# Kernel optimization log

Measured on AMD Instinct MI355X. Metric: run time of the kernel, lower is better.

Reference implementation:

```python
import jax, jax.numpy as jnp
import numpy as np
import math

INF = 10000000000.0
D_KEY = 64


def setup_inputs() -> dict:
    key = jax.random.key(0)
    kq, kk, kv = jax.random.split(key, 3)
    B, S, D = 4, 4096, D_KEY
    return {
        "query": jax.random.normal(kq, (B, S, D), dtype=jnp.float32),
        "key": jax.random.normal(kk, (B, S, D), dtype=jnp.float32),
        "value": jax.random.normal(kv, (B, S, D), dtype=jnp.float32),
    }


def reference(query, key, value):
    # dot_products: [B, Sq, Sk]
    scale = math.sqrt(D_KEY)
    scores = jnp.einsum("bqd,bkd->bqk", query, key)
    S = key.shape[1]
    # causal: subtract INF on strict upper triangle (triu(1)), before scaling
    tri = jnp.triu(jnp.full((S, S), INF, dtype=scores.dtype), k=1)
    scores = scores - tri[None, :, :]
    logits = scores / scale
    probs = jax.nn.softmax(logits, axis=-1)  # softmax over key dim
    # dropout p=0.0 -> identity
    return jnp.einsum("bqk,bkd->bqd", probs, value)
```

## Files before the change

### kernel.cpp

```cpp
#include <hip/hip_runtime.h>
#include <hip/hip_bf16.h>
#include <math.h>

#define B_  4
#define S_  4096
#define D_  64
#define NQT 64
#define NST 32
#define LDP 68
#define QSC 0.18033688f
#define M0  20.0f

typedef __attribute__((ext_vector_type(8))) short bf16x8;
typedef __attribute__((ext_vector_type(4))) float f32x4;
typedef __attribute__((ext_vector_type(4))) short short4v;

static __device__ inline short f2bf(float f) {
    union { float f; unsigned u; } v; v.f = f;
    unsigned u = v.u;
    unsigned r = u + 0x7fff + ((u >> 16) & 1);
    return (short)(r >> 16);
}
static __device__ inline float bf2f(short s) {
    union { unsigned u; float f; } v; v.u = ((unsigned)(unsigned short)s) << 16;
    return v.f;
}

__global__ __launch_bounds__(256) void fa_prep(const float* __restrict__ K,
                                               const float* __restrict__ V,
                                               short* __restrict__ Kbf,
                                               short* __restrict__ Vtbf)
{
    const int b   = blockIdx.x >> 6;
    const int st  = blockIdx.x & 63;
    const int tid = threadIdx.x;
    __shared__ short Vs[64 * 72];

    const size_t tbase = ((size_t)b * S_ + (size_t)st * 64) * D_;
    #pragma unroll
    for (int rr = 0; rr < 4; ++rr) {
        int i = tid + rr * 256;
        size_t e = tbase + (size_t)i * 4;
        f32x4 k = *(const f32x4*)(K + e);
        short4v ks;
        ks[0] = f2bf(k[0]); ks[1] = f2bf(k[1]);
        ks[2] = f2bf(k[2]); ks[3] = f2bf(k[3]);
        *(short4v*)(Kbf + e) = ks;
        f32x4 v = *(const f32x4*)(V + e);
        int key = i >> 4, d4 = (i & 15) * 4;
        Vs[(d4 + 0) * 72 + key] = f2bf(v[0]);
        Vs[(d4 + 1) * 72 + key] = f2bf(v[1]);
        Vs[(d4 + 2) * 72 + key] = f2bf(v[2]);
        Vs[(d4 + 3) * 72 + key] = f2bf(v[3]);
    }
    __syncthreads();
    #pragma unroll
    for (int cc = 0; cc < 2; ++cc) {
        int c = tid + cc * 256;
        int d = c >> 3, sg = c & 7;
        bf16x8 row = *(const bf16x8*)&Vs[d * 72 + sg * 8];
        *(bf16x8*)(Vtbf + ((size_t)(b * D_ + d)) * S_ + (size_t)st * 64 + sg * 8) = row;
    }
}

__global__ __launch_bounds__(512) void fa_part(const float* __restrict__ Qf,
                                               const short* __restrict__ Kbf,
                                               const short* __restrict__ Vtbf,
                                               short* __restrict__ Opart,
                                               float* __restrict__ Lpart,
                                               int CH, int T)
{
    const int bid = blockIdx.x;
    const int b   = bid / T;
    int r = bid - b * T;
    int qt2 = NST - 1;
    while (true) {
        int n = (2 * qt2 + 2 + CH - 1) / CH;
        if (r < n) break;
        r -= n; --qt2;
    }
    const int kt0 = r * CH;
    const int nkt = 2 * qt2 + 2;
    const int kt1 = (kt0 + CH < nkt) ? kt0 + CH : nkt;

    const int tid  = threadIdx.x;
    const int wave = tid >> 6;
    const int lane = tid & 63;
    const int lm   = lane & 15;
    const int lk   = lane >> 4;

    __shared__ __align__(16) short Ks[64 * 64];
    __shared__ __align__(16) short Vt[64 * 64];
    __shared__ __align__(16) short Ps[128 * LDP];

    bf16x8 qA[2];
    {
        const float* qp = Qf + ((size_t)(b * S_ + qt2 * 128 + wave * 16 + lm)) * D_;
        #pragma unroll
        for (int h = 0; h < 2; ++h) {
            f32x4 a0 = *(const f32x4*)(qp + h * 32 + lk * 8);
            f32x4 a1 = *(const f32x4*)(qp + h * 32 + lk * 8 + 4);
            qA[h][0] = f2bf(a0[0] * QSC); qA[h][1] = f2bf(a0[1] * QSC);
            qA[h][2] = f2bf(a0[2] * QSC); qA[h][3] = f2bf(a0[3] * QSC);
            qA[h][4] = f2bf(a1[0] * QSC); qA[h][5] = f2bf(a1[1] * QSC);
            qA[h][6] = f2bf(a1[2] * QSC); qA[h][7] = f2bf(a1[3] * QSC);
        }
    }

    const int srow = tid >> 3;
    const int sseg = (tid & 7) ^ (srow & 7);
    const char* kgp = (const char*)(Kbf + (size_t)b * S_ * D_)
                    + (size_t)(kt0 * 64 + srow) * 128 + sseg * 16;
    const char* vgp = (const char*)(Vtbf + ((size_t)(b * D_ + srow)) * S_)
                    + (size_t)kt0 * 128 + sseg * 16;

    bf16x8 kreg = *(const bf16x8*)kgp;
    bf16x8 vreg = *(const bf16x8*)vgp;
    kgp += 8192; vgp += 128;

    float l_i[4] = {0.f, 0.f, 0.f, 0.f};
    f32x4 o_acc[4];
    #pragma unroll
    for (int dt = 0; dt < 4; ++dt) o_acc[dt] = (f32x4){0.f, 0.f, 0.f, 0.f};

    const int wrow = wave * 16 + lk * 4;

    for (int kt = kt0; kt < kt1; ++kt) {
        __syncthreads();
        *(bf16x8*)&Ks[tid * 8] = kreg;
        *(bf16x8*)&Vt[tid * 8] = vreg;
        __syncthreads();

        if (kt + 1 < kt1) {
            kreg = *(const bf16x8*)kgp;
            vreg = *(const bf16x8*)vgp;
            kgp += 8192; vgp += 128;
        }

        f32x4 s4[4];
        #pragma unroll
        for (int ct = 0; ct < 4; ++ct) {
            f32x4 acc = (f32x4){0.f, 0.f, 0.f, 0.f};
            #pragma unroll
            for (int h = 0; h < 2; ++h) {
                int seg = (h * 4 + lk) ^ (lm & 7);
                bf16x8 bF = *(const bf16x8*)&Ks[(ct * 16 + lm) * 64 + seg * 8];
                acc = __builtin_amdgcn_mfma_f32_16x16x32_bf16(qA[h], bF, acc, 0, 0, 0);
            }
            s4[ct] = acc;
        }

        if (kt >= 2 * qt2) {
            const int koff = kt * 64 - qt2 * 128;
            #pragma unroll
            for (int ct = 0; ct < 4; ++ct) {
                #pragma unroll
                for (int rr = 0; rr < 4; ++rr) {
                    if (koff + ct * 16 + lm > wrow + rr) s4[ct][rr] = -INFINITY;
                }
            }
        }

        #pragma unroll
        for (int ct = 0; ct < 4; ++ct) {
            #pragma unroll
            for (int rr = 0; rr < 4; ++rr) {
                float p = exp2f(s4[ct][rr] - M0);
                s4[ct][rr] = p;
                l_i[rr] += p;
            }
        }
        #pragma unroll
        for (int ct = 0; ct < 4; ++ct) {
            #pragma unroll
            for (int rr = 0; rr < 4; ++rr) {
                Ps[(wrow + rr) * LDP + ct * 16 + lm] = f2bf(s4[ct][rr]);
            }
        }
        bf16x8 aF[2];
        #pragma unroll
        for (int kh = 0; kh < 2; ++kh)
            aF[kh] = *(const bf16x8*)&Ps[(wave * 16 + lm) * LDP + kh * 32 + lk * 8];
        #pragma unroll
        for (int dt = 0; dt < 4; ++dt) {
            #pragma unroll
            for (int kh = 0; kh < 2; ++kh) {
                int seg = (kh * 4 + lk) ^ (lm & 7);
                bf16x8 bF = *(const bf16x8*)&Vt[(dt * 16 + lm) * 64 + seg * 8];
                o_acc[dt] = __builtin_amdgcn_mfma_f32_16x16x32_bf16(aF[kh], bF, o_acc[dt], 0, 0, 0);
            }
        }
    }

    short* Op = Opart + (size_t)bid * (128 * D_);
    #pragma unroll
    for (int rr = 0; rr < 4; ++rr) {
        float rs = l_i[rr];
        rs += __shfl_xor(rs, 1);
        rs += __shfl_xor(rs, 2);
        rs += __shfl_xor(rs, 4);
        rs += __shfl_xor(rs, 8);
        int row = wrow + rr;
        #pragma unroll
        for (int dt = 0; dt < 4; ++dt)
            Op[row * D_ + dt * 16 + lm] = f2bf(o_acc[dt][rr]);
        if (lm == 0) Lpart[(size_t)bid * 128 + row] = rs;
    }
}

__global__ __launch_bounds__(256) void fa_combine(const short* __restrict__ Opart,
                                                  const float* __restrict__ Lpart,
                                                  float* __restrict__ O,
                                                  int CH, int T)
{
    const int idx = blockIdx.x * 256 + threadIdx.x;
    const int b   = idx / (S_ * 16);
    const int rem = idx - b * (S_ * 16);
    const int q   = rem >> 4;
    const int d4  = (rem & 15) << 2;
    const int qt2 = q >> 7;
    const int rit = q & 127;

    int F = 0;
    for (int y = qt2 + 1; y < NST; ++y) F += (2 * y + 2 + CH - 1) / CH;
    const int base = b * T + F;
    const int nch  = (2 * qt2 + 2 + CH - 1) / CH;

    float L = 0.f;
    f32x4 acc = (f32x4){0.f, 0.f, 0.f, 0.f};
    for (int c = 0; c < nch; ++c) {
        L += Lpart[(size_t)(base + c) * 128 + rit];
        short4v o = *(const short4v*)(Opart + (size_t)(base + c) * (128 * D_) + rit * D_ + d4);
        acc[0] += bf2f(o[0]); acc[1] += bf2f(o[1]);
        acc[2] += bf2f(o[2]); acc[3] += bf2f(o[3]);
    }
    float inv = 1.f / L;
    f32x4 outv;
    outv[0] = acc[0] * inv; outv[1] = acc[1] * inv;
    outv[2] = acc[2] * inv; outv[3] = acc[3] * inv;
    *(f32x4*)(O + (size_t)idx * 4) = outv;
}

__global__ __launch_bounds__(256) void fa_fwd(const float* __restrict__ Q,
                                              const float* __restrict__ K,
                                              const float* __restrict__ V,
                                              float* __restrict__ O)
{
    const int qt   = (gridDim.x - 1) - blockIdx.x;
    const int b    = blockIdx.y;
    const int tid  = threadIdx.x;
    const int wave = tid >> 6;
    const int lane = tid & 63;
    const int lm   = lane & 15;
    const int lk   = lane >> 4;

    __shared__ short Ks[64 * 72];
    __shared__ short Vt[64 * 72];
    __shared__ short Ps[64 * 72];

    const float* Qb = Q + ((size_t)b * S_ + (size_t)qt * 64) * D_;
    const float* Kb = K + (size_t)b * S_ * D_;
    const float* Vb = V + (size_t)b * S_ * D_;

    bf16x8 qA[2];
    {
        const float* qp = Qb + (wave * 16 + lm) * D_;
        #pragma unroll
        for (int h = 0; h < 2; ++h) {
            const float* p = qp + h * 32 + lk * 8;
            #pragma unroll
            for (int j = 0; j < 8; ++j) qA[h][j] = f2bf(p[j] * 0.125f);
        }
    }
    float m_i[4], l_i[4];
    f32x4 o_acc[4];
    #pragma unroll
    for (int rr = 0; rr < 4; ++rr) { m_i[rr] = -INFINITY; l_i[rr] = 0.f; }
    #pragma unroll
    for (int dt = 0; dt < 4; ++dt) o_acc[dt] = (f32x4){0.f, 0.f, 0.f, 0.f};

    const int n_kt = qt + 1;
    for (int kt = 0; kt < n_kt; ++kt) {
        __syncthreads();
        #pragma unroll
        for (int rr = 0; rr < 4; ++rr) {
            int i   = tid + rr * 256;
            int row = i >> 4;
            int c4  = (i & 15) * 4;
            const size_t gbase = ((size_t)(kt * 64 + row)) * D_ + c4;
            f32x4 kv = *(const f32x4*)(Kb + gbase);
            short4v ks;
            ks[0] = f2bf(kv[0]); ks[1] = f2bf(kv[1]);
            ks[2] = f2bf(kv[2]); ks[3] = f2bf(kv[3]);
            *(short4v*)&Ks[row * 72 + c4] = ks;
            f32x4 vv = *(const f32x4*)(Vb + gbase);
            Vt[(c4 + 0) * 72 + row] = f2bf(vv[0]);
            Vt[(c4 + 1) * 72 + row] = f2bf(vv[1]);
            Vt[(c4 + 2) * 72 + row] = f2bf(vv[2]);
            Vt[(c4 + 3) * 72 + row] = f2bf(vv[3]);
        }
        __syncthreads();
        f32x4 s4[4];
        #pragma unroll
        for (int ct = 0; ct < 4; ++ct) {
            f32x4 acc = (f32x4){0.f, 0.f, 0.f, 0.f};
            #pragma unroll
            for (int h = 0; h < 2; ++h) {
                bf16x8 bF = *(const bf16x8*)&Ks[(ct * 16 + lm) * 72 + h * 32 + lk * 8];
                acc = __builtin_amdgcn_mfma_f32_16x16x32_bf16(qA[h], bF, acc, 0, 0, 0);
            }
            s4[ct] = acc;
        }
        if (kt == qt) {
            #pragma unroll
            for (int ct = 0; ct < 4; ++ct) {
                #pragma unroll
                for (int rr = 0; rr < 4; ++rr) {
                    int qrow = wave * 16 + lk * 4 + rr;
                    int kcol = ct * 16 + lm;
                    if (kcol > qrow) s4[ct][rr] = -INFINITY;
                }
            }
        }
        float alpha[4];
        #pragma unroll
        for (int rr = 0; rr < 4; ++rr) {
            float mx = fmaxf(fmaxf(s4[0][rr], s4[1][rr]), fmaxf(s4[2][rr], s4[3][rr]));
            mx = fmaxf(mx, __shfl_xor(mx, 1));
            mx = fmaxf(mx, __shfl_xor(mx, 2));
            mx = fmaxf(mx, __shfl_xor(mx, 4));
            mx = fmaxf(mx, __shfl_xor(mx, 8));
            float mn = fmaxf(m_i[rr], mx);
            alpha[rr] = __expf(m_i[rr] - mn);
            m_i[rr] = mn;
        }
        float rsum[4] = {0.f, 0.f, 0.f, 0.f};
        #pragma unroll
        for (int ct = 0; ct < 4; ++ct) {
            #pragma unroll
            for (int rr = 0; rr < 4; ++rr) {
                float p = __expf(s4[ct][rr] - m_i[rr]);
                s4[ct][rr] = p;
                rsum[rr] += p;
            }
        }
        #pragma unroll
        for (int rr = 0; rr < 4; ++rr) {
            float rs = rsum[rr];
            rs += __shfl_xor(rs, 1);
            rs += __shfl_xor(rs, 2);
            rs += __shfl_xor(rs, 4);
            rs += __shfl_xor(rs, 8);
            l_i[rr] = l_i[rr] * alpha[rr] + rs;
        }
        #pragma unroll
        for (int ct = 0; ct < 4; ++ct) {
            #pragma unroll
            for (int rr = 0; rr < 4; ++rr) {
                Ps[(wave * 16 + lk * 4 + rr) * 72 + ct * 16 + lm] = f2bf(s4[ct][rr]);
            }
        }
        #pragma unroll
        for (int dt = 0; dt < 4; ++dt) {
            #pragma unroll
            for (int rr = 0; rr < 4; ++rr) o_acc[dt][rr] *= alpha[rr];
        }
        #pragma unroll
        for (int dt = 0; dt < 4; ++dt) {
            #pragma unroll
            for (int kh = 0; kh < 2; ++kh) {
                bf16x8 aF = *(const bf16x8*)&Ps[(wave * 16 + lm) * 72 + kh * 32 + lk * 8];
                bf16x8 bF = *(const bf16x8*)&Vt[(dt * 16 + lm) * 72 + kh * 32 + lk * 8];
                o_acc[dt] = __builtin_amdgcn_mfma_f32_16x16x32_bf16(aF, bF, o_acc[dt], 0, 0, 0);
            }
        }
    }
    float* Ob = O + ((size_t)b * S_ + (size_t)qt * 64) * D_;
    #pragma unroll
    for (int rr = 0; rr < 4; ++rr) {
        float inv = 1.f / l_i[rr];
        int row = wave * 16 + lk * 4 + rr;
        #pragma unroll
        for (int dt = 0; dt < 4; ++dt) {
            Ob[row * D_ + dt * 16 + lm] = o_acc[dt][rr] * inv;
        }
    }
}

extern "C" void kernel_launch(void* const* d_in, const int* in_sizes, int n_in,
                              void* d_out, int out_size, void* d_ws, size_t ws_size,
                              hipStream_t stream) {
    const float* Q = (const float*)d_in[0];
    const float* K = (const float*)d_in[1];
    const float* V = (const float*)d_in[2];
    float* O = (float*)d_out;

    const size_t convShorts = (size_t)B_ * S_ * D_;
    int CH = 0, T = 0;
    const int chs[5] = {4, 8, 16, 32, 64};
    for (int k = 0; k < 5; ++k) {
        int c = chs[k];
        int t = 0;
        for (int q2 = 0; q2 < NST; ++q2) t += (2 * q2 + 2 + c - 1) / c;
        size_t need = 2 * convShorts * 2
                    + (size_t)B_ * t * (128 * D_) * 2
                    + (size_t)B_ * t * 128 * 4;
        if (need <= ws_size) { CH = c; T = t; break; }
    }
    if (CH == 0) {
        dim3 grid(NQT, B_);
        fa_fwd<<<grid, 256, 0, stream>>>(Q, K, V, O);
        return;
    }
    short* Kbf   = (short*)d_ws;
    short* Vtbf  = Kbf + convShorts;
    short* Opart = Vtbf + convShorts;
    float* Lpart = (float*)(Opart + (size_t)B_ * T * (128 * D_));

    fa_prep<<<dim3(B_ * NQT), 256, 0, stream>>>(K, V, Kbf, Vtbf);
    fa_part<<<dim3(B_ * T), 512, 0, stream>>>(Q, Kbf, Vtbf, Opart, Lpart, CH, T);
    fa_combine<<<dim3((B_ * S_ * 16) / 256), 256, 0, stream>>>(Opart, Lpart, O, CH, T);
}
```

Before: 101.5 us.

## Fuse split-K combine into partial kernel via atomic last-block reduction

Result: slower. 203.0 us (+100.0%).

```diff
diff --git a/kernel.cpp b/kernel.cpp
--- a/kernel.cpp
+++ b/kernel.cpp
@@ -10,6 +10,9 @@
 #define LDP 68
 #define QSC 0.18033688f
 #define M0  20.0f
+#define CHQ 16
+#define TQ  80
+#define NBLK (B_ * TQ)
 
 typedef __attribute__((ext_vector_type(8))) short bf16x8;
 typedef __attribute__((ext_vector_type(4))) float f32x4;
@@ -68,30 +71,36 @@
                                                const short* __restrict__ Vtbf,
                                                short* __restrict__ Opart,
                                                float* __restrict__ Lpart,
-                                               int CH, int T)
+                                               int* __restrict__ cnt,
+                                               float* __restrict__ O)
 {
     const int bid = blockIdx.x;
-    const int b   = bid / T;
-    int r = bid - b * T;
+    const int b   = bid / TQ;
+    int r = bid - b * TQ;
     int qt2 = NST - 1;
+    int F = 0;
     while (true) {
-        int n = (2 * qt2 + 2 + CH - 1) / CH;
+        int n = (2 * qt2 + 2 + CHQ - 1) / CHQ;
         if (r < n) break;
-        r -= n; --qt2;
-    }
-    const int kt0 = r * CH;
+        r -= n; --qt2; F += n;
+    }
+    const int kt0 = r * CHQ;
     const int nkt = 2 * qt2 + 2;
-    const int kt1 = (kt0 + CH < nkt) ? kt0 + CH : nkt;
+    const int kt1 = (kt0 + CHQ < nkt) ? kt0 + CHQ : nkt;
+    const int nch = (nkt + CHQ - 1) / CHQ;
+    const int base = b * TQ + F;
 
     const int tid  = threadIdx.x;
     const int wave = tid >> 6;
     const int lane = tid & 63;
     const int lm   = lane & 15;
     const int lk   = lane >> 4;
+    const int wrow = wave * 16 + lk * 4;
 
     __shared__ __align__(16) short Ks[64 * 64];
     __shared__ __align__(16) short Vt[64 * 64];
     __shared__ __align__(16) short Ps[128 * LDP];
+    __shared__ int oldv;
 
     bf16x8 qA[2];
     {
@@ -123,8 +132,6 @@
     #pragma unroll
     for (int dt = 0; dt < 4; ++dt) o_acc[dt] = (f32x4){0.f, 0.f, 0.f, 0.f};
 
-    const int wrow = wave * 16 + lk * 4;
-
     for (int kt = kt0; kt < kt1; ++kt) {
         __syncthreads();
         *(bf16x8*)&Ks[tid * 8] = kreg;
@@ -192,7 +199,7 @@
         }
     }
 
-    short* Op = Opart + (size_t)bid * (128 * D_);
+    float rsum[4];
     #pragma unroll
     for (int rr = 0; rr < 4; ++rr) {
         float rs = l_i[rr];
@@ -200,45 +207,58 @@
         rs += __shfl_xor(rs, 2);
         rs += __shfl_xor(rs, 4);
         rs += __shfl_xor(rs, 8);
+        rsum[rr] = rs;
+    }
+
+    if (nch == 1) {
+        float* Ob = O + ((size_t)(b * S_ + qt2 * 128)) * D_;
+        #pragma unroll
+        for (int rr = 0; rr < 4; ++rr) {
+            float inv = 1.f / rsum[rr];
+            int row = wrow + rr;
+            #pragma unroll
+            for (int dt = 0; dt < 4; ++dt)
+                Ob[row * D_ + dt * 16 + lm] = o_acc[dt][rr] * inv;
+        }
+        return;
+    }
+
+    short* Op = Opart + (size_t)bid * (128 * D_);
+    #pragma unroll
+    for (int rr = 0; rr < 4; ++rr) {
         int row = wrow + rr;
         #pragma unroll
         for (int dt = 0; dt < 4; ++dt)
             Op[row * D_ + dt * 16 + lm] = f2bf(o_acc[dt][rr]);
-        if (lm == 0) Lpart[(size_t)bid * 128 + row] = rs;
-    }
-}
-
-__global__ __launch_bounds__(256) void fa_combine(const short* __restrict__ Opart,
-                                                  const float* __restrict__ Lpart,
-                                                  float* __restrict__ O,
-                                                  int CH, int T)
-{
-    const int idx = blockIdx.x * 256 + threadIdx.x;
-    const int b   = idx / (S_ * 16);
-    const int rem = idx - b * (S_ * 16);
-    const int q   = rem >> 4;
-    const int d4  = (rem & 15) << 2;
-    const int qt2 = q >> 7;
-    const int rit = q & 127;
-
-    int F = 0;
-    for (int y = qt2 + 1; y < NST; ++y) F += (2 * y + 2 + CH - 1) / CH;
-    const int base = b * T + F;
-    const int nch  = (2 * qt2 + 2 + CH - 1) / CH;
-
-    float L = 0.f;
-    f32x4 acc = (f32x4){0.f, 0.f, 0.f, 0.f};
-    for (int c = 0; c < nch; ++c) {
-        L += Lpart[(size_t)(base + c) * 128 + rit];
-        short4v o = *(const short4v*)(Opart + (size_t)(base + c) * (128 * D_) + rit * D_ + d4);
-        acc[0] += bf2f(o[0]); acc[1] += bf2f(o[1]);
-        acc[2] += bf2f(o[2]); acc[3] += bf2f(o[3]);
-    }
-    float inv = 1.f / L;
-    f32x4 outv;
-    outv[0] = acc[0] * inv; outv[1] = acc[1] * inv;
-    outv[2] = acc[2] * inv; outv[3] = acc[3] * inv;
-    *(f32x4*)(O + (size_t)idx * 4) = outv;
+        if (lm == 0) Lpart[(size_t)bid * 128 + row] = rsum[rr];
+    }
+
+    __threadfence();
+    __syncthreads();
+    if (tid == 0)
+        oldv = __hip_atomic_fetch_add(&cnt[b * NST + qt2], 1,
+                                      __ATOMIC_ACQ_REL, __HIP_MEMORY_SCOPE_AGENT);
+    __syncthreads();
+    if (oldv != nch - 1) return;
+
+    __threadfence();
+    for (int u = tid; u < 2048; u += 512) {
+        const int rit = u >> 4;
+        const int d4  = (u & 15) << 2;
+        float L = 0.f;
+        f32x4 acc = (f32x4){0.f, 0.f, 0.f, 0.f};
+        for (int c = 0; c < nch; ++c) {
+            L += Lpart[(size_t)(base + c) * 128 + rit];
+            short4v o = *(const short4v*)(Opart + (size_t)(base + c) * (128 * D_) + rit * D_ + d4);
+            acc[0] += bf2f(o[0]); acc[1] += bf2f(o[1]);
+            acc[2] += bf2f(o[2]); acc[3] += bf2f(o[3]);
+        }
+        float inv = 1.f / L;
+        f32x4 outv;
+        outv[0] = acc[0] * inv; outv[1] = acc[1] * inv;
+        outv[2] = acc[2] * inv; outv[3] = acc[3] * inv;
+        *(f32x4*)(O + ((size_t)(b * S_ + qt2 * 128 + rit)) * D_ + d4) = outv;
+    }
 }
 
 __global__ __launch_bounds__(256) void fa_fwd(const float* __restrict__ Q,
@@ -396,28 +416,24 @@
     float* O = (float*)d_out;
 
     const size_t convShorts = (size_t)B_ * S_ * D_;
-    int CH = 0, T = 0;
-    const int chs[5] = {4, 8, 16, 32, 64};
-    for (int k = 0; k < 5; ++k) {
-        int c = chs[k];
-        int t = 0;
-        for (int q2 = 0; q2 < NST; ++q2) t += (2 * q2 + 2 + c - 1) / c;
-        size_t need = 2 * convShorts * 2
-                    + (size_t)B_ * t * (128 * D_) * 2
-                    + (size_t)B_ * t * 128 * 4;
-        if (need <= ws_size) { CH = c; T = t; break; }
-    }
-    if (CH == 0) {
+    const size_t cntBytes = 512;
+    const size_t need = cntBytes
+                      + 2 * convShorts * 2
+                      + (size_t)NBLK * (128 * D_) * 2
+                      + (size_t)NBLK * 128 * 4;
+    if (need > ws_size) {
         dim3 grid(NQT, B_);
         fa_fwd<<<grid, 256, 0, stream>>>(Q, K, V, O);
         return;
     }
-    short* Kbf   = (short*)d_ws;
+
+    int*   cnt   = (int*)d_ws;
+    short* Kbf   = (short*)((char*)d_ws + cntBytes);
     short* Vtbf  = Kbf + convShorts;
     short* Opart = Vtbf + convShorts;
-    float* Lpart = (float*)(Opart + (size_t)B_ * T * (128 * D_));
-
+    float* Lpart = (float*)(Opart + (size_t)NBLK * (128 * D_));
+
+    hipMemsetAsync(cnt, 0, cntBytes, stream);
     fa_prep<<<dim3(B_ * NQT), 256, 0, stream>>>(K, V, Kbf, Vtbf);
-    fa_part<<<dim3(B_ * T), 512, 0, stream>>>(Q, Kbf, Vtbf, Opart, Lpart, CH, T);
-    fa_combine<<<dim3((B_ * S_ * 16) / 256), 256, 0, stream>>>(Opart, Lpart, O, CH, T);
-}
+    fa_part<<<dim3(NBLK), 512, 0, stream>>>(Q, Kbf, Vtbf, Opart, Lpart, cnt, O);
+}
```
